# Optimization experiments

Hardware: AMD Instinct MI355X
Metric: run time of the kernel (lower is better)

Reference implementation:

```python
import jax, jax.numpy as jnp
import numpy as np

N_NODES = 50000
N_EDGES = 800000
IN_C, HID_C, OUT_C = 128, 128, 64
BN_EPS = 1e-5


def _normalized_adj(edge_index, N):
    # Mirrors remove_self_loops + add_self_loops + symmetric GCN normalization.
    src, dst = edge_index[0], edge_index[1]
    mask = (src != dst).astype(jnp.float32)  # drop original self loops
    # degree of dst over (masked edges + added self loops)
    deg = jax.ops.segment_sum(mask, dst, num_segments=N) + 1.0
    dinv = jnp.where(deg > 0, deg ** -0.5, 0.0)
    w = mask * dinv[src] * dinv[dst]          # weights for original edges
    w_self = dinv * dinv                      # weights for added self loops
    return src, dst, w, w_self


def _spmm(src, dst, w, w_self, x):
    # torch.sparse.mm(adj, x): out[i] = sum_{e: src[e]=i} w[e] * x[dst[e]] + w_self[i]*x[i]
    agg = jax.ops.segment_sum(w[:, None] * x[dst], src, num_segments=x.shape[0])
    return agg + w_self[:, None] * x


def setup_inputs() -> dict:
    key = jax.random.key(0)
    ks = jax.random.split(key, 4)
    x = jax.random.normal(ks[0], (N_NODES, IN_C), dtype=jnp.float32)
    edge_index = jax.random.randint(ks[1], (2, N_EDGES), 0, N_NODES, dtype=jnp.int64)
    # glorot init for GCN linear weights
    s1 = np.sqrt(6.0 / (IN_C + HID_C)).astype(np.float32)
    s2 = np.sqrt(6.0 / (HID_C + OUT_C)).astype(np.float32)
    W1 = jax.random.uniform(ks[2], (IN_C, HID_C), jnp.float32, -s1, s1)
    W2 = jax.random.uniform(ks[3], (HID_C, OUT_C), jnp.float32, -s2, s2)
    return {
        "x": x,
        "edge_index": edge_index,
        "W1": W1,
        "b1": jnp.zeros((HID_C,), jnp.float32),
        "gamma": jnp.ones((HID_C,), jnp.float32),
        "beta": jnp.zeros((HID_C,), jnp.float32),
        "W2": W2,
        "b2": jnp.zeros((OUT_C,), jnp.float32),
    }


def reference(x, edge_index, W1, b1, gamma, beta, W2, b2):
    N = x.shape[0]
    src, dst, w, w_self = _normalized_adj(edge_index, N)
    # layer 1: linear -> SpMM -> BN (batch stats) -> ReLU (dropout: eval)
    h = x @ W1 + b1
    h = _spmm(src, dst, w, w_self, h)
    mean = h.mean(axis=0)
    var = jnp.mean((h - mean) ** 2, axis=0)
    h = (h - mean) * jax.lax.rsqrt(var + BN_EPS) * gamma + beta
    h = jax.nn.relu(h)
    # layer 2: linear -> SpMM
    h = h @ W2 + b2
    h = _spmm(src, dst, w, w_self, h)
    return h
```

## Files before the change

### kernel.cpp

```cpp
#include <hip/hip_runtime.h>

#define N_NODES 50000
#define N_EDGES 800000
#define BN_EPS 1e-5f
#define NPAD 50176
#define SCAN_BLOCKS 98

#define S_SLICES 64
#define R_RANGES 4
#define BINS 16384
#define NP4 (R_RANGES * BINS)
#define ES (N_EDGES / S_SLICES)

#define XS_STRIDE 68

typedef unsigned int uint;
typedef unsigned short ushort;
typedef unsigned char uchar;
typedef float floatx4 __attribute__((ext_vector_type(4)));
typedef short bf16x8 __attribute__((ext_vector_type(8)));

__device__ __forceinline__ float bfl(uint u) { return __uint_as_float(u << 16); }
__device__ __forceinline__ float bfh(uint u) { return __uint_as_float(u & 0xffff0000u); }
__device__ __forceinline__ uint pack_bf2(float a, float b) {
    uint ua = __float_as_uint(a), ub = __float_as_uint(b);
    ua += 0x7fffu + ((ua >> 16) & 1u);
    ub += 0x7fffu + ((ub >> 16) & 1u);
    return (ua >> 16) | (ub & 0xffff0000u);
}
__device__ __forceinline__ ushort bf1(float x) {
    uint u = __float_as_uint(x);
    u += 0x7fffu + ((u >> 16) & 1u);
    return (ushort)(u >> 16);
}
__device__ __forceinline__ void acc8(float* a, uint4 h, float w) {
    a[0] += w * bfl(h.x); a[1] += w * bfh(h.x);
    a[2] += w * bfl(h.y); a[3] += w * bfh(h.y);
    a[4] += w * bfl(h.z); a[5] += w * bfh(h.z);
    a[6] += w * bfl(h.w); a[7] += w * bfh(h.w);
}

__global__ __launch_bounds__(256) void count_hist_kernel(const int* __restrict__ src,
                                                         const int* __restrict__ dst,
                                                         const float* __restrict__ W1,
                                                         const float* __restrict__ W2,
                                                         uint* __restrict__ W1t,
                                                         uint* __restrict__ W2t,
                                                         uchar* __restrict__ part_cnt,
                                                         uchar* __restrict__ part_deg) {
    if (blockIdx.x == S_SLICES * R_RANGES) {
        for (int t = threadIdx.x; t < 12288; t += 256) {
            if (t < 8192) {
                int n = t >> 6, kk = t & 63;
                W1t[t] = pack_bf2(W1[(2 * kk) * 128 + n], W1[(2 * kk + 1) * 128 + n]);
            } else {
                int u = t - 8192;
                int n = u >> 6, kk = u & 63;
                W2t[u] = pack_bf2(W2[(2 * kk) * 64 + n], W2[(2 * kk + 1) * 64 + n]);
            }
        }
        return;
    }
    __shared__ uint cnt_lds[BINS / 4];
    __shared__ uint deg_lds[BINS / 4];
    const int s = blockIdx.x / R_RANGES;
    const int r = blockIdx.x % R_RANGES;
    const int base = r * BINS;
    for (int j = threadIdx.x; j < BINS / 4; j += 256) { cnt_lds[j] = 0u; deg_lds[j] = 0u; }
    __syncthreads();
    const int4* s4 = (const int4*)(src + s * ES);
    const int4* d4 = (const int4*)(dst + s * ES);
#pragma unroll 2
    for (int g = threadIdx.x; g < ES / 4; g += 256) {
        int4 sv = s4[g];
        int4 dv = d4[g];
#pragma unroll
        for (int k = 0; k < 4; ++k) {
            int ss = (&sv.x)[k], dd = (&dv.x)[k];
            if (ss != dd) {
                int a = ss - base;
                if ((unsigned)a < (unsigned)BINS)
                    atomicAdd(&cnt_lds[a >> 2], 1u << ((a & 3) * 8));
                int b = dd - base;
                if ((unsigned)b < (unsigned)BINS)
                    atomicAdd(&deg_lds[b >> 2], 1u << ((b & 3) * 8));
            }
        }
    }
    __syncthreads();
    uint* pc = (uint*)&part_cnt[s * NP4 + base];
    uint* pd = (uint*)&part_deg[s * NP4 + base];
    for (int j = threadIdx.x; j < BINS / 4; j += 256) { pc[j] = cnt_lds[j]; pd[j] = deg_lds[j]; }
}

__global__ __launch_bounds__(256) void reduce_scan_kernel(const uchar* __restrict__ part_deg,
                                                          const uchar* __restrict__ part_cnt,
                                                          float* __restrict__ dinv,
                                                          int* __restrict__ rowcnt,
                                                          int* __restrict__ rowptr,
                                                          int* __restrict__ psum,
                                                          float* __restrict__ stats) {
    const int t = threadIdx.x;
    if (blockIdx.x == 0) stats[t] = 0.f;
    const int i = blockIdx.x * 512 + 2 * t;
    uint dg0 = 0, dg1 = 0, rc0 = 0, rc1 = 0;
#pragma unroll 8
    for (int s = 0; s < S_SLICES; ++s) {
        uint vd = *(const ushort*)&part_deg[s * NP4 + i];
        uint vc = *(const ushort*)&part_cnt[s * NP4 + i];
        dg0 += vd & 0xffu; dg1 += vd >> 8;
        rc0 += vc & 0xffu; rc1 += vc >> 8;
    }
    *(int2*)&rowcnt[i] = make_int2((int)rc0, (int)rc1);
    if (i < N_NODES) dinv[i] = rsqrtf((float)dg0 + 1.0f);
    if (i + 1 < N_NODES) dinv[i + 1] = rsqrtf((float)dg1 + 1.0f);

    __shared__ int bs[256];
    const int pair = (int)(rc0 + rc1);
    bs[t] = pair;
    __syncthreads();
#pragma unroll
    for (int off = 1; off < 256; off <<= 1) {
        int x = (t >= off) ? bs[t - off] : 0;
        __syncthreads();
        bs[t] += x;
        __syncthreads();
    }
    const int excl = bs[t] - pair;
    *(int2*)&rowptr[i] = make_int2(excl + (int)rc0, excl + pair);
    if (t == 255) psum[blockIdx.x] = bs[255];
}

__global__ __launch_bounds__(256) void cursor_init_kernel(const int* __restrict__ rowcnt,
                                                          int* __restrict__ rowptr,
                                                          const int* __restrict__ psum,
                                                          const uchar* __restrict__ part_cnt,
                                                          int* __restrict__ cursor) {
    __shared__ int pbuf[SCAN_BLOCKS];
    __shared__ int lps;
    const int t = threadIdx.x;
    if (t < SCAN_BLOCKS) pbuf[t] = psum[t];
    __syncthreads();
    if (t == 0) {
        int acc = 0;
        for (int j = 0; j < (int)blockIdx.x; ++j) acc += pbuf[j];
        lps = acc;
    }
    __syncthreads();
    const int ps = lps;
    const int i = blockIdx.x * 512 + 2 * t;
    int b0 = rowptr[i] - rowcnt[i] + ps;
    int b1 = rowptr[i + 1] - rowcnt[i + 1] + ps;
    *(int2*)&rowptr[i] = make_int2(b0, b1);
#pragma unroll 8
    for (int s = 0; s < S_SLICES; ++s) {
        *(int2*)&cursor[s * NP4 + i] = make_int2(b0, b1);
        uint vc = *(const ushort*)&part_cnt[s * NP4 + i];
        b0 += (int)(vc & 0xffu);
        b1 += (int)(vc >> 8);
    }
}

__global__ __launch_bounds__(256) void fill_lds_kernel(const int* __restrict__ src,
                                                       const int* __restrict__ dst,
                                                       const float* __restrict__ dinv,
                                                       const int* __restrict__ cursor,
                                                       int2* __restrict__ epair) {
    __shared__ int curs[BINS];
    const int s = blockIdx.x / R_RANGES;
    const int r = blockIdx.x % R_RANGES;
    const int base = r * BINS;
    const int* gc = &cursor[s * NP4 + base];
    for (int j = threadIdx.x; j < BINS; j += 256) curs[j] = gc[j];
    __syncthreads();
    const int4* s4 = (const int4*)(src + s * ES);
    const int4* d4 = (const int4*)(dst + s * ES);
#pragma unroll 2
    for (int g = threadIdx.x; g < ES / 4; g += 256) {
        int4 sv = s4[g];
        int4 dv = d4[g];
#pragma unroll
        for (int k = 0; k < 4; ++k) {
            int ss = (&sv.x)[k], dd = (&dv.x)[k];
            int a = ss - base;
            if (ss != dd && (unsigned)a < (unsigned)BINS) {
                int pos = atomicAdd(&curs[a], 1);
                epair[pos] = make_int2(dd, __float_as_int(dinv[ss] * dinv[dd]));
            }
        }
    }
}

__global__ __launch_bounds__(256) void gemm1_mfma_kernel(const float* __restrict__ X,
                                                         const uint* __restrict__ W1t,
                                                         const float* __restrict__ bias,
                                                         ushort* __restrict__ Hbf) {
    __shared__ uint lds[(64 + 128) * XS_STRIDE];
    uint* Xs = lds;
    uint* Ws = lds + 64 * XS_STRIDE;
    const int t = threadIdx.x;
    const int rowBase = blockIdx.x * 64;

    {
        int r = t >> 2, q = t & 3;
        int arow = rowBase + r;
        uint* xd = &Xs[r * XS_STRIDE + q * 16];
        if (arow < N_NODES) {
            const float4* xp = (const float4*)&X[arow * 128 + q * 32];
#pragma unroll
            for (int i = 0; i < 8; ++i) {
                float4 v = xp[i];
                xd[2 * i]     = pack_bf2(v.x, v.y);
                xd[2 * i + 1] = pack_bf2(v.z, v.w);
            }
        } else {
#pragma unroll
            for (int i = 0; i < 16; ++i) xd[i] = 0u;
        }
    }
    {
        int n = t >> 1, half = t & 1;
        const uint4* wp = (const uint4*)&W1t[n * 64 + half * 32];
        uint* wd = &Ws[n * XS_STRIDE + half * 32];
#pragma unroll
        for (int i = 0; i < 8; ++i) *(uint4*)&wd[i * 4] = wp[i];
    }
    __syncthreads();

    const int wv = t >> 6, lane = t & 63;
    const int lr = lane & 15;
    const int ko = (lane >> 4) * 4;
    const int m0 = wv * 16;
    floatx4 acc[8];
#pragma unroll
    for (int j = 0; j < 8; ++j) acc[j] = (floatx4){0.f, 0.f, 0.f, 0.f};

#pragma unroll
    for (int ks = 0; ks < 4; ++ks) {
        const int kb = ks * 16 + ko;
        bf16x8 a = *(bf16x8*)&Xs[(m0 + lr) * XS_STRIDE + kb];
#pragma unroll
        for (int j = 0; j < 8; ++j) {
            bf16x8 b = *(bf16x8*)&Ws[(j * 16 + lr) * XS_STRIDE + kb];
            acc[j] = __builtin_amdgcn_mfma_f32_16x16x32_bf16(a, b, acc[j], 0, 0, 0);
        }
    }
    const int rbase = rowBase + m0 + (lane >> 4) * 4;
#pragma unroll
    for (int j = 0; j < 8; ++j) {
        const int col = j * 16 + lr;
        const float bb = bias[col];
#pragma unroll
        for (int r = 0; r < 4; ++r) {
            int row = rbase + r;
            if (row < N_NODES) Hbf[row * 128 + col] = bf1(acc[j][r] + bb);
        }
    }
}

__global__ __launch_bounds__(256) void gemm2_mfma_kernel(const uint* __restrict__ Hin,
                                                         const uint* __restrict__ W2t,
                                                         const float* __restrict__ bias,
                                                         const float* __restrict__ sum,
                                                         const float* __restrict__ sumsq,
                                                         const float* __restrict__ gamma,
                                                         const float* __restrict__ beta,
                                                         ushort* __restrict__ Hbf) {
    __shared__ uint lds[(64 + 64) * XS_STRIDE];
    __shared__ float sc_sh[128], sh_sh[128];
    uint* Xs = lds;
    uint* Ws = lds + 64 * XS_STRIDE;
    const int t = threadIdx.x;
    const int rowBase = blockIdx.x * 64;

    if (t < 128) {
        float mean = sum[t] * (1.0f / N_NODES);
        float var = sumsq[t] * (1.0f / N_NODES) - mean * mean;
        float sc = gamma[t] * rsqrtf(var + BN_EPS);
        sc_sh[t] = sc;
        sh_sh[t] = beta[t] - mean * sc;
    }
    if (t >= 128) {
        int u = t - 128;
        int n = u >> 1, half = u & 1;
        const uint4* wp = (const uint4*)&W2t[n * 64 + half * 32];
        uint* wd = &Ws[n * XS_STRIDE + half * 32];
#pragma unroll
        for (int i = 0; i < 8; ++i) *(uint4*)&wd[i * 4] = wp[i];
    }
    __syncthreads();

    {
        int r = t >> 2, q = t & 3;
        int arow = rowBase + r;
        uint* xd = &Xs[r * XS_STRIDE + q * 16];
        if (arow < N_NODES) {
            const uint* hp = &Hin[arow * 64 + q * 16];
#pragma unroll
            for (int i = 0; i < 16; ++i) {
                uint u = hp[i];
                int m = q * 16 + i;
                float a0 = fmaxf(0.f, bfl(u) * sc_sh[2 * m] + sh_sh[2 * m]);
                float a1 = fmaxf(0.f, bfh(u) * sc_sh[2 * m + 1] + sh_sh[2 * m + 1]);
                xd[i] = pack_bf2(a0, a1);
            }
        } else {
#pragma unroll
            for (int i = 0; i < 16; ++i) xd[i] = 0u;
        }
    }
    __syncthreads();

    const int wv = t >> 6, lane = t & 63;
    const int lr = lane & 15;
    const int ko = (lane >> 4) * 4;
    const int m0 = wv * 16;
    floatx4 acc[4];
#pragma unroll
    for (int j = 0; j < 4; ++j) acc[j] = (floatx4){0.f, 0.f, 0.f, 0.f};

#pragma unroll
    for (int ks = 0; ks < 4; ++ks) {
        const int kb = ks * 16 + ko;
        bf16x8 a = *(bf16x8*)&Xs[(m0 + lr) * XS_STRIDE + kb];
#pragma unroll
        for (int j = 0; j < 4; ++j) {
            bf16x8 b = *(bf16x8*)&Ws[(j * 16 + lr) * XS_STRIDE + kb];
            acc[j] = __builtin_amdgcn_mfma_f32_16x16x32_bf16(a, b, acc[j], 0, 0, 0);
        }
    }
    const int rbase = rowBase + m0 + (lane >> 4) * 4;
#pragma unroll
    for (int j = 0; j < 4; ++j) {
        const int col = j * 16 + lr;
        const float bb = bias[col];
#pragma unroll
        for (int r = 0; r < 4; ++r) {
            int row = rbase + r;
            if (row < N_NODES) Hbf[row * 64 + col] = bf1(acc[j][r] + bb);
        }
    }
}

template <int C, bool OUT_BF16>
__global__ __launch_bounds__(256) void spmm_bf16_kernel(const int* __restrict__ rowptr,
                                                        const int2* __restrict__ epair,
                                                        const float* __restrict__ dinv,
                                                        const uint* __restrict__ H,
                                                        void* __restrict__ outv) {
    constexpr int LPR = C / 8;
    constexpr int RPB = 256 / LPR;
    constexpr int US  = C / 2;
    const int t = threadIdx.x;
    const int lane = t % LPR;
    const int row = blockIdx.x * RPB + t / LPR;
    if (row >= N_NODES) return;
    const int cu = lane * 4;
    const float di = dinv[row];

    float acc[8];
    {
        uint4 hv = *(const uint4*)&H[row * US + cu];
        float w = di * di;
        acc[0] = w * bfl(hv.x); acc[1] = w * bfh(hv.x);
        acc[2] = w * bfl(hv.y); acc[3] = w * bfh(hv.y);
        acc[4] = w * bfl(hv.z); acc[5] = w * bfh(hv.z);
        acc[6] = w * bfl(hv.w); acc[7] = w * bfh(hv.w);
    }
    const int e0 = rowptr[row], e1 = rowptr[row + 1];
    int e = e0;
    if ((e & 1) && e < e1) {
        int2 p = epair[e];
        uint4 h = *(const uint4*)&H[p.x * US + cu];
        acc8(acc, h, __int_as_float(p.y));
        ++e;
    }
    const int4* ep4 = (const int4*)epair;
    for (; e + 8 <= e1; e += 8) {
        int4 qa = ep4[(e >> 1) + 0];
        int4 qb = ep4[(e >> 1) + 1];
        int4 qc = ep4[(e >> 1) + 2];
        int4 qd = ep4[(e >> 1) + 3];
        uint4 h0 = *(const uint4*)&H[qa.x * US + cu];
        uint4 h1 = *(const uint4*)&H[qa.z * US + cu];
        uint4 h2 = *(const uint4*)&H[qb.x * US + cu];
        uint4 h3 = *(const uint4*)&H[qb.z * US + cu];
        uint4 h4 = *(const uint4*)&H[qc.x * US + cu];
        uint4 h5 = *(const uint4*)&H[qc.z * US + cu];
        uint4 h6 = *(const uint4*)&H[qd.x * US + cu];
        uint4 h7 = *(const uint4*)&H[qd.z * US + cu];
        acc8(acc, h0, __int_as_float(qa.y));
        acc8(acc, h1, __int_as_float(qa.w));
        acc8(acc, h2, __int_as_float(qb.y));
        acc8(acc, h3, __int_as_float(qb.w));
        acc8(acc, h4, __int_as_float(qc.y));
        acc8(acc, h5, __int_as_float(qc.w));
        acc8(acc, h6, __int_as_float(qd.y));
        acc8(acc, h7, __int_as_float(qd.w));
    }
    for (; e + 2 <= e1; e += 2) {
        int4 q = ep4[e >> 1];
        uint4 h0 = *(const uint4*)&H[q.x * US + cu];
        uint4 h1 = *(const uint4*)&H[q.z * US + cu];
        acc8(acc, h0, __int_as_float(q.y));
        acc8(acc, h1, __int_as_float(q.w));
    }
    if (e < e1) {
        int2 p = epair[e];
        uint4 h = *(const uint4*)&H[p.x * US + cu];
        acc8(acc, h, __int_as_float(p.y));
    }
    if (OUT_BF16) {
        uint4 o;
        o.x = pack_bf2(acc[0], acc[1]);
        o.y = pack_bf2(acc[2], acc[3]);
        o.z = pack_bf2(acc[4], acc[5]);
        o.w = pack_bf2(acc[6], acc[7]);
        *(uint4*)&((uint*)outv)[row * US + cu] = o;
    } else {
        float* out = (float*)outv;
        *(float4*)&out[row * C + lane * 8]     = make_float4(acc[0], acc[1], acc[2], acc[3]);
        *(float4*)&out[row * C + lane * 8 + 4] = make_float4(acc[4], acc[5], acc[6], acc[7]);
    }
}

__global__ __launch_bounds__(256) void bn_stats_kernel(const uint* __restrict__ H,
                                                       float* __restrict__ sum,
                                                       float* __restrict__ sumsq) {
    int uc = threadIdx.x & 63;
    int quarter = threadIdx.x >> 6;
    float s0 = 0.f, q0 = 0.f, s1 = 0.f, q1 = 0.f;
    for (int r = blockIdx.x * 4 + quarter; r < N_NODES; r += 512) {
        uint u = H[r * 64 + uc];
        float a = bfl(u), b = bfh(u);
        s0 += a; q0 += a * a;
        s1 += b; q1 += b * b;
    }
    __shared__ float red[4][256];
    red[0][threadIdx.x] = s0; red[1][threadIdx.x] = q0;
    red[2][threadIdx.x] = s1; red[3][threadIdx.x] = q1;
    __syncthreads();
    if (quarter == 0) {
        float ts0 = 0.f, tq0 = 0.f, ts1 = 0.f, tq1 = 0.f;
#pragma unroll
        for (int k = 0; k < 4; ++k) {
            ts0 += red[0][k * 64 + uc]; tq0 += red[1][k * 64 + uc];
            ts1 += red[2][k * 64 + uc]; tq1 += red[3][k * 64 + uc];
        }
        atomicAdd(&sum[2 * uc], ts0);
        atomicAdd(&sum[2 * uc + 1], ts1);
        atomicAdd(&sumsq[2 * uc], tq0);
        atomicAdd(&sumsq[2 * uc + 1], tq1);
    }
}

extern "C" void kernel_launch(void* const* d_in, const int* in_sizes, int n_in,
                              void* d_out, int out_size, void* d_ws, size_t ws_size,
                              hipStream_t stream) {
    const float* x     = (const float*)d_in[0];
    const int*   ei    = (const int*)d_in[1];
    const float* W1    = (const float*)d_in[2];
    const float* b1    = (const float*)d_in[3];
    const float* gamma = (const float*)d_in[4];
    const float* beta  = (const float*)d_in[5];
    const float* W2    = (const float*)d_in[6];
    const float* b2    = (const float*)d_in[7];
    float* out = (float*)d_out;
    const int* src = ei;
    const int* dst = ei + N_EDGES;

    float* ws     = (float*)d_ws;
    float* dinv   = ws;
    float* stats  = ws + NPAD;
    int*   psum   = (int*)(ws + NPAD + 512);
    int*   rowcnt = psum + 128;
    int*   rowptr = rowcnt + NPAD;
    float* big    = (float*)(rowptr + NPAD);
    int2*   epair    = (int2*)big;
    uchar*  part_cnt = (uchar*)(big + 1600000);
    uchar*  part_deg = (uchar*)(big + 3700000);
    int*    cursor   = (int*)(big + 5800000);
    ushort* h1bf     = (ushort*)(big + 1600000);
    uint*   h1agg    = (uint*)(big + 4800000);
    ushort* h2bf     = h1bf;
    uint*   W1t      = (uint*)(big + 10000000);
    uint*   W2t      = W1t + 8192;
    float* sum    = stats;
    float* sumsq  = stats + 128;

    count_hist_kernel<<<S_SLICES * R_RANGES + 1, 256, 0, stream>>>(src, dst, W1, W2, W1t, W2t,
                                                                   part_cnt, part_deg);
    reduce_scan_kernel<<<SCAN_BLOCKS, 256, 0, stream>>>(part_deg, part_cnt, dinv, rowcnt,
                                                        rowptr, psum, stats);
    cursor_init_kernel<<<SCAN_BLOCKS, 256, 0, stream>>>(rowcnt, rowptr, psum, part_cnt, cursor);
    fill_lds_kernel<<<S_SLICES * R_RANGES, 256, 0, stream>>>(src, dst, dinv, cursor, epair);

    gemm1_mfma_kernel<<<(N_NODES + 63) / 64, 256, 0, stream>>>(x, W1t, b1, h1bf);

    spmm_bf16_kernel<128, true><<<(N_NODES + 15) / 16, 256, 0, stream>>>(
        rowptr, epair, dinv, (const uint*)h1bf, (void*)h1agg);

    bn_stats_kernel<<<128, 256, 0, stream>>>(h1agg, sum, sumsq);

    gemm2_mfma_kernel<<<(N_NODES + 63) / 64, 256, 0, stream>>>(h1agg, W2t, b2, sum, sumsq,
                                                               gamma, beta, h2bf);

    spmm_bf16_kernel<64, false><<<(N_NODES + 31) / 32, 256, 0, stream>>>(
        rowptr, epair, dinv, (const uint*)h2bf, (void*)out);
}
```

Measured before the change: 243.3 us.

## Fuse CSR fill with gemm1, store ushort cursors, split SpMM rows across two thread groups

Three changes. The cursor kernel now writes 16-bit per-slice prefix offsets instead of full int cursors, and the fill step adds rowptr back in when it loads them into LDS, which cuts cursor write and read traffic. The fill and gemm1 kernels are merged into one launch, with block ranges selecting the role, so the two independent jobs can run side by side and one launch goes away. The SpMM kernel gives each row two thread groups that take alternating edge pairs and combine results with a cross-lane shuffle, doubling parallelism per row at the cost of more blocks and a reduction step; the row-range guard is removed because N_NODES divides evenly by the new rows-per-block.

```diff
diff --git a/kernel.cpp b/kernel.cpp
--- a/kernel.cpp
+++ b/kernel.cpp
@@ -13,6 +13,9 @@
 #define ES (N_EDGES / S_SLICES)
 
 #define XS_STRIDE 68
+
+#define NB_FILL (S_SLICES * R_RANGES)
+#define NB_G1   ((N_NODES + 63) / 64)
 
 typedef unsigned int uint;
 typedef unsigned short ushort;
@@ -48,7 +51,7 @@
                                                          uint* __restrict__ W2t,
                                                          uchar* __restrict__ part_cnt,
                                                          uchar* __restrict__ part_deg) {
-    if (blockIdx.x == S_SLICES * R_RANGES) {
+    if (blockIdx.x == NB_FILL) {
         for (int t = threadIdx.x; t < 12288; t += 256) {
             if (t < 8192) {
                 int n = t >> 6, kk = t & 63;
@@ -135,7 +138,7 @@
                                                           int* __restrict__ rowptr,
                                                           const int* __restrict__ psum,
                                                           const uchar* __restrict__ part_cnt,
-                                                          int* __restrict__ cursor) {
+                                                          ushort* __restrict__ pre) {
     __shared__ int pbuf[SCAN_BLOCKS];
     __shared__ int lps;
     const int t = threadIdx.x;
@@ -152,54 +155,63 @@
     int b0 = rowptr[i] - rowcnt[i] + ps;
     int b1 = rowptr[i + 1] - rowcnt[i + 1] + ps;
     *(int2*)&rowptr[i] = make_int2(b0, b1);
+    uint p0 = 0, p1 = 0;
 #pragma unroll 8
     for (int s = 0; s < S_SLICES; ++s) {
-        *(int2*)&cursor[s * NP4 + i] = make_int2(b0, b1);
+        *(ushort2*)&pre[s * NP4 + i] = make_ushort2((ushort)p0, (ushort)p1);
         uint vc = *(const ushort*)&part_cnt[s * NP4 + i];
-        b0 += (int)(vc & 0xffu);
-        b1 += (int)(vc >> 8);
-    }
-}
-
-__global__ __launch_bounds__(256) void fill_lds_kernel(const int* __restrict__ src,
-                                                       const int* __restrict__ dst,
-                                                       const float* __restrict__ dinv,
-                                                       const int* __restrict__ cursor,
-                                                       int2* __restrict__ epair) {
-    __shared__ int curs[BINS];
-    const int s = blockIdx.x / R_RANGES;
-    const int r = blockIdx.x % R_RANGES;
-    const int base = r * BINS;
-    const int* gc = &cursor[s * NP4 + base];
-    for (int j = threadIdx.x; j < BINS; j += 256) curs[j] = gc[j];
-    __syncthreads();
-    const int4* s4 = (const int4*)(src + s * ES);
-    const int4* d4 = (const int4*)(dst + s * ES);
-#pragma unroll 2
-    for (int g = threadIdx.x; g < ES / 4; g += 256) {
-        int4 sv = s4[g];
-        int4 dv = d4[g];
-#pragma unroll
-        for (int k = 0; k < 4; ++k) {
-            int ss = (&sv.x)[k], dd = (&dv.x)[k];
-            int a = ss - base;
-            if (ss != dd && (unsigned)a < (unsigned)BINS) {
-                int pos = atomicAdd(&curs[a], 1);
-                epair[pos] = make_int2(dd, __float_as_int(dinv[ss] * dinv[dd]));
-            }
-        }
-    }
-}
-
-__global__ __launch_bounds__(256) void gemm1_mfma_kernel(const float* __restrict__ X,
+        p0 += vc & 0xffu;
+        p1 += vc >> 8;
+    }
+}
+
+__global__ __launch_bounds__(256) void fill_gemm1_kernel(const int* __restrict__ src,
+                                                         const int* __restrict__ dst,
+                                                         const float* __restrict__ dinv,
+                                                         const int* __restrict__ rowptr,
+                                                         const ushort* __restrict__ pre,
+                                                         int2* __restrict__ epair,
+                                                         const float* __restrict__ X,
                                                          const uint* __restrict__ W1t,
                                                          const float* __restrict__ bias,
                                                          ushort* __restrict__ Hbf) {
-    __shared__ uint lds[(64 + 128) * XS_STRIDE];
-    uint* Xs = lds;
-    uint* Ws = lds + 64 * XS_STRIDE;
+    __shared__ uint smem[BINS];
     const int t = threadIdx.x;
-    const int rowBase = blockIdx.x * 64;
+
+    if (blockIdx.x < NB_FILL) {
+        int* curs = (int*)smem;
+        const int s = blockIdx.x / R_RANGES;
+        const int r = blockIdx.x % R_RANGES;
+        const int base = r * BINS;
+        const ushort* pr = &pre[s * NP4 + base];
+        for (int j = t; j < BINS; j += 256) {
+            int node = base + j;
+            int rp = (node < NPAD) ? rowptr[node] : 0;
+            curs[j] = rp + (int)pr[j];
+        }
+        __syncthreads();
+        const int4* s4 = (const int4*)(src + s * ES);
+        const int4* d4 = (const int4*)(dst + s * ES);
+#pragma unroll 2
+        for (int g = t; g < ES / 4; g += 256) {
+            int4 sv = s4[g];
+            int4 dv = d4[g];
+#pragma unroll
+            for (int k = 0; k < 4; ++k) {
+                int ss = (&sv.x)[k], dd = (&dv.x)[k];
+                int a = ss - base;
+                if (ss != dd && (unsigned)a < (unsigned)BINS) {
+                    int pos = atomicAdd(&curs[a], 1);
+                    epair[pos] = make_int2(dd, __float_as_int(dinv[ss] * dinv[dd]));
+                }
+            }
+        }
+        return;
+    }
+
+    uint* Xs = smem;
+    uint* Ws = smem + 64 * XS_STRIDE;
+    const int rowBase = (blockIdx.x - NB_FILL) * 64;
 
     {
         int r = t >> 2, q = t & 3;
@@ -349,38 +361,49 @@
                                                         const uint* __restrict__ H,
                                                         void* __restrict__ outv) {
     constexpr int LPR = C / 8;
-    constexpr int RPB = 256 / LPR;
+    constexpr int TPR = LPR * 2;
+    constexpr int RPB = 256 / TPR;
     constexpr int US  = C / 2;
     const int t = threadIdx.x;
     const int lane = t % LPR;
-    const int row = blockIdx.x * RPB + t / LPR;
-    if (row >= N_NODES) return;
+    const int g = (t / LPR) & 1;
+    const int row = blockIdx.x * RPB + t / TPR;
     const int cu = lane * 4;
-    const float di = dinv[row];
 
     float acc[8];
-    {
+#pragma unroll
+    for (int j = 0; j < 8; ++j) acc[j] = 0.f;
+    if (g == 0) {
+        const float di = dinv[row];
         uint4 hv = *(const uint4*)&H[row * US + cu];
-        float w = di * di;
-        acc[0] = w * bfl(hv.x); acc[1] = w * bfh(hv.x);
-        acc[2] = w * bfl(hv.y); acc[3] = w * bfh(hv.y);
-        acc[4] = w * bfl(hv.z); acc[5] = w * bfh(hv.z);
-        acc[6] = w * bfl(hv.w); acc[7] = w * bfh(hv.w);
+        acc8(acc, hv, di * di);
     }
     const int e0 = rowptr[row], e1 = rowptr[row + 1];
-    int e = e0;
-    if ((e & 1) && e < e1) {
-        int2 p = epair[e];
-        uint4 h = *(const uint4*)&H[p.x * US + cu];
-        acc8(acc, h, __int_as_float(p.y));
-        ++e;
+    int lo = e0, hi = e1;
+    if (lo & 1) {
+        if (g == 0 && lo < hi) {
+            int2 p = epair[lo];
+            uint4 h = *(const uint4*)&H[p.x * US + cu];
+            acc8(acc, h, __int_as_float(p.y));
+        }
+        ++lo;
+    }
+    if (lo < hi && (hi & 1)) {
+        --hi;
+        if (g == 1) {
+            int2 p = epair[hi];
+            uint4 h = *(const uint4*)&H[p.x * US + cu];
+            acc8(acc, h, __int_as_float(p.y));
+        }
     }
     const int4* ep4 = (const int4*)epair;
-    for (; e + 8 <= e1; e += 8) {
-        int4 qa = ep4[(e >> 1) + 0];
-        int4 qb = ep4[(e >> 1) + 1];
-        int4 qc = ep4[(e >> 1) + 2];
-        int4 qd = ep4[(e >> 1) + 3];
+    int p = (lo >> 1) + g;
+    const int pe = hi >> 1;
+    for (; p + 6 < pe; p += 8) {
+        int4 qa = ep4[p + 0];
+        int4 qb = ep4[p + 2];
+        int4 qc = ep4[p + 4];
+        int4 qd = ep4[p + 6];
         uint4 h0 = *(const uint4*)&H[qa.x * US + cu];
         uint4 h1 = *(const uint4*)&H[qa.z * US + cu];
         uint4 h2 = *(const uint4*)&H[qb.x * US + cu];
@@ -398,18 +421,16 @@
         acc8(acc, h6, __int_as_float(qd.y));
         acc8(acc, h7, __int_as_float(qd.w));
     }
-    for (; e + 2 <= e1; e += 2) {
-        int4 q = ep4[e >> 1];
+    for (; p < pe; p += 2) {
+        int4 q = ep4[p];
         uint4 h0 = *(const uint4*)&H[q.x * US + cu];
         uint4 h1 = *(const uint4*)&H[q.z * US + cu];
         acc8(acc, h0, __int_as_float(q.y));
         acc8(acc, h1, __int_as_float(q.w));
     }
-    if (e < e1) {
-        int2 p = epair[e];
-        uint4 h = *(const uint4*)&H[p.x * US + cu];
-        acc8(acc, h, __int_as_float(p.y));
-    }
+#pragma unroll
+    for (int j = 0; j < 8; ++j) acc[j] += __shfl_xor(acc[j], LPR, 64);
+    if (g != 0) return;
     if (OUT_BF16) {
         uint4 o;
         o.x = pack_bf2(acc[0], acc[1]);
@@ -479,7 +500,7 @@
     int2*   epair    = (int2*)big;
     uchar*  part_cnt = (uchar*)(big + 1600000);
     uchar*  part_deg = (uchar*)(big + 3700000);
-    int*    cursor   = (int*)(big + 5800000);
+    ushort* pre      = (ushort*)(big + 5800000);
     ushort* h1bf     = (ushort*)(big + 1600000);
     uint*   h1agg    = (uint*)(big + 4800000);
     ushort* h2bf     = h1bf;
@@ -488,16 +509,16 @@
     float* sum    = stats;
     float* sumsq  = stats + 128;
 
-    count_hist_kernel<<<S_SLICES * R_RANGES + 1, 256, 0, stream>>>(src, dst, W1, W2, W1t, W2t,
-                                                                   part_cnt, part_deg);
+    count_hist_kernel<<<NB_FILL + 1, 256, 0, stream>>>(src, dst, W1, W2, W1t, W2t,
+                                                       part_cnt, part_deg);
     reduce_scan_kernel<<<SCAN_BLOCKS, 256, 0, stream>>>(part_deg, part_cnt, dinv, rowcnt,
                                                         rowptr, psum, stats);
-    cursor_init_kernel<<<SCAN_BLOCKS, 256, 0, stream>>>(rowcnt, rowptr, psum, part_cnt, cursor);
-    fill_lds_kernel<<<S_SLICES * R_RANGES, 256, 0, stream>>>(src, dst, dinv, cursor, epair);
-
-    gemm1_mfma_kernel<<<(N_NODES + 63) / 64, 256, 0, stream>>>(x, W1t, b1, h1bf);
-
-    spmm_bf16_kernel<128, true><<<(N_NODES + 15) / 16, 256, 0, stream>>>(
+    cursor_init_kernel<<<SCAN_BLOCKS, 256, 0, stream>>>(rowcnt, rowptr, psum, part_cnt, pre);
+
+    fill_gemm1_kernel<<<NB_FILL + NB_G1, 256, 0, stream>>>(src, dst, dinv, rowptr, pre, epair,
+                                                           x, W1t, b1, h1bf);
+
+    spmm_bf16_kernel<128, true><<<N_NODES / 8, 256, 0, stream>>>(
         rowptr, epair, dinv, (const uint*)h1bf, (void*)h1agg);
 
     bn_stats_kernel<<<128, 256, 0, stream>>>(h1agg, sum, sumsq);
@@ -505,6 +526,6 @@
     gemm2_mfma_kernel<<<(N_NODES + 63) / 64, 256, 0, stream>>>(h1agg, W2t, b2, sum, sumsq,
                                                                gamma, beta, h2bf);
 
-    spmm_bf16_kernel<64, false><<<(N_NODES + 31) / 32, 256, 0, stream>>>(
+    spmm_bf16_kernel<64, false><<<N_NODES / 16, 256, 0, stream>>>(
         rowptr, epair, dinv, (const uint*)h2bf, (void*)out);
 }
```

After: 249.1 us. 1.02x slower.
